# Performance work log

Hardware: AMD Instinct MI355X
Metric: run time of the kernel (lower is better)

Reference implementation:

```python
import jax, jax.numpy as jnp
import numpy as np

N = 10000      # nodes
E = 100000     # edges per direction
DIN = 128      # input feature dim (== hidden so layers stack)
H = 4          # attention heads
C = 128        # out channels per head (concat=False -> mean over heads)
ED = 16        # edge_attr dim
L = 2          # number of layers (len(hidden_sizes))
NEG_SLOPE = 0.2
EPS = 1e-5


def setup_inputs() -> dict:
    key = jax.random.key(0)
    ks = jax.random.split(key, 32)
    f32 = jnp.float32

    def nrm(k, shape, s=0.05):
        return jax.random.normal(k, shape, dtype=f32) * s

    inp = {}
    inp["x"] = nrm(ks[0], (N, DIN), 1.0)
    inp["fwd_edges_index"] = jax.random.randint(ks[1], (2, E), 0, N, dtype=jnp.int32)
    inp["bwd_edges_index"] = jax.random.randint(ks[2], (2, E), 0, N, dtype=jnp.int32)
    inp["edge_attr"] = nrm(ks[3], (E, ED), 1.0)
    # GATv2 params, stacked over layers; suffix _f = FWDGATLayer, _b = BWDGATLayer
    for i, sfx in enumerate(["f", "b"]):
        o = 4 + 7 * i
        inp[f"Wl_{sfx}"] = nrm(ks[o + 0], (L, DIN, H * C))   # lin_l (source x_j)
        inp[f"bl_{sfx}"] = jnp.zeros((L, H * C), f32)
        inp[f"Wr_{sfx}"] = nrm(ks[o + 1], (L, DIN, H * C))   # lin_r (target x_i)
        inp[f"br_{sfx}"] = jnp.zeros((L, H * C), f32)
        inp[f"We_{sfx}"] = nrm(ks[o + 2], (L, ED, H * C))    # lin_edge (no bias)
        inp[f"att_{sfx}"] = nrm(ks[o + 3], (L, H, C))        # attention vector a
        inp[f"bias_{sfx}"] = jnp.zeros((L, C), f32)          # final bias (concat=False)
    # Merge MLP: Linear(2C,C) -> ReLU -> Linear(C,C)
    inp["Wm1"] = nrm(ks[20], (L, 2 * C, C)); inp["bm1"] = jnp.zeros((L, C), f32)
    inp["Wm2"] = nrm(ks[21], (L, C, C));     inp["bm2"] = jnp.zeros((L, C), f32)
    # BatchNorm affine params (training-mode batch stats)
    inp["gamma"] = jnp.ones((L, C), f32)
    inp["beta"] = jnp.zeros((L, C), f32)
    return inp


def gatv2(x, src, dst, eattr, Wl, bl, Wr, br, We, att, bias):
    """PyG GATv2Conv, heads=H, concat=False (mean over heads), share_weights=False."""
    xl = (x @ Wl + bl).reshape(N, H, C)          # source-side transform (x_j)
    xr = (x @ Wr + br).reshape(N, H, C)          # target-side transform (x_i)
    ee = (eattr @ We).reshape(E, H, C)           # edge embedding
    z = jax.nn.leaky_relu(xl[src] + xr[dst] + ee, NEG_SLOPE)   # [E,H,C]
    logits = jnp.einsum('ehc,hc->eh', z, att)    # per-edge per-head scores
    # scatter-softmax over incoming edges of each target node
    amax = jax.lax.stop_gradient(jax.ops.segment_max(logits, dst, num_segments=N))
    amax = jnp.where(jnp.isfinite(amax), amax, 0.0)  # nodes with no in-edges
    ex = jnp.exp(logits - amax[dst])
    denom = jax.ops.segment_sum(ex, dst, num_segments=N)
    alpha = ex / denom[dst]                      # [E,H]
    msg = (xl[src] * alpha[:, :, None]).reshape(E, H * C)
    agg = jax.ops.segment_sum(msg, dst, num_segments=N).reshape(N, H, C)
    return agg.mean(axis=1) + bias               # concat=False -> head mean


def batch_norm(x, gamma, beta):
    mu = x.mean(axis=0)
    var = x.var(axis=0)  # biased var, as torch BN uses for normalization
    return gamma * (x - mu) * jax.lax.rsqrt(var + EPS) + beta


def reference(x, fwd_edges_index, bwd_edges_index, edge_attr,
              Wl_f, bl_f, Wr_f, br_f, We_f, att_f, bias_f,
              Wl_b, bl_b, Wr_b, br_b, We_b, att_b, bias_b,
              Wm1, bm1, Wm2, bm2, gamma, beta):
    fs, fd = fwd_edges_index[0], fwd_edges_index[1]
    bs, bd = bwd_edges_index[0], bwd_edges_index[1]
    h = x
    for l in range(L):
        f = gatv2(h, fs, fd, edge_attr, Wl_f[l], bl_f[l], Wr_f[l], br_f[l],
                  We_f[l], att_f[l], bias_f[l])
        b = gatv2(h, bs, bd, edge_attr, Wl_b[l], bl_b[l], Wr_b[l], br_b[l],
                  We_b[l], att_b[l], bias_b[l])
        m = jnp.concatenate([f, b], axis=1)                     # [N, 2C]
        m = jax.nn.relu(m @ Wm1[l] + bm1[l]) @ Wm2[l] + bm2[l]  # merge MLP
        h = jax.nn.relu(batch_norm(m, gamma[l], beta[l]))
    return h
```

## Files before the change

kernel.cpp:

```cpp
#include <hip/hip_runtime.h>

constexpr int N_  = 10000;
constexpr int E_  = 100000;
constexpr int HC_ = 512;
constexpr int MP_ = 10112;
constexpr float NEG_SLOPE_ = 0.2f;

typedef unsigned int u32;
typedef unsigned short u16;
typedef __attribute__((ext_vector_type(8))) short bf16x8;
typedef __attribute__((ext_vector_type(4))) float f32x4;

__device__ __forceinline__ u16 f2bf(float f) {
  u32 u = __float_as_uint(f);
  u32 r = u + 0x7fffu + ((u >> 16) & 1u);
  return (u16)(r >> 16);
}
__device__ __forceinline__ float bf2f(u16 u) {
  return __uint_as_float((u32)u << 16);
}
__device__ __forceinline__ void async16(const void* g, void* l) {
  __builtin_amdgcn_global_load_lds((const __attribute__((address_space(1))) u32*)g,
                                   (__attribute__((address_space(3))) u32*)l, 16, 0, 0);
}


__global__ void k_hist(const int* __restrict__ fdst, const int* __restrict__ bdst,
                       int* __restrict__ degf, int* __restrict__ degb) {
  int e = blockIdx.x * 256 + threadIdx.x;
  if (e < E_) {
    atomicAdd(&degf[fdst[e]], 1);
    atomicAdd(&degb[bdst[e]], 1);
  }
}

__global__ void k_scan(const int* __restrict__ degf, const int* __restrict__ degb,
                       int* __restrict__ rpf, int* __restrict__ rpb) {
  const int* deg = blockIdx.x ? degb : degf;
  int* rp = blockIdx.x ? rpb : rpf;
  const int CH = 40;
  int t = threadIdx.x;
  int base = t * CH;
  int s = 0;
  for (int i = 0; i < CH; ++i) {
    int idx = base + i;
    if (idx < N_) s += deg[idx];
  }
  __shared__ int lds[256];
  lds[t] = s;
  __syncthreads();
  for (int off = 1; off < 256; off <<= 1) {
    int v = (t >= off) ? lds[t - off] : 0;
    __syncthreads();
    lds[t] += v;
    __syncthreads();
  }
  int run = lds[t] - s;
  for (int i = 0; i < CH; ++i) {
    int idx = base + i;
    if (idx < N_) { rp[idx] = run; run += deg[idx]; }
  }
  if (t == 255) rp[N_] = lds[255];
}

__global__ void k_scatter(const int* __restrict__ src, const int* __restrict__ dst,
                          const int* __restrict__ rp, int* __restrict__ cur,
                          int* __restrict__ csrc, int* __restrict__ ceid) {
  int e = blockIdx.x * 256 + threadIdx.x;
  if (e < E_) {
    int d = dst[e];
    int pos = rp[d] + atomicAdd(&cur[d], 1);
    csrc[pos] = src[e];
    ceid[pos] = e;
  }
}


__global__ void k_wprep(const float* __restrict__ Wl_f, const float* __restrict__ Wr_f,
                        const float* __restrict__ Wl_b, const float* __restrict__ Wr_b,
                        const float* __restrict__ bl_f, const float* __restrict__ br_f,
                        const float* __restrict__ bl_b, const float* __restrict__ br_b,
                        const float* __restrict__ Wm1, const float* __restrict__ Wm2,
                        u16* __restrict__ WCATh, float* __restrict__ BCAT,
                        u16* __restrict__ WM1h, u16* __restrict__ WM2h) {
  int idx = blockIdx.x * 256 + threadIdx.x;
  if (idx < 2 * 2048 * 128) {
    int l = idx >> 18;
    int rem = idx & 262143;
    int j = rem >> 7, k = rem & 127;
    int grp = j >> 9, jj = j & 511;
    const float* W = grp == 0 ? Wl_f : grp == 1 ? Wr_f : grp == 2 ? Wl_b : Wr_b;
    WCATh[idx] = f2bf(W[((size_t)(l * 128 + k)) * 512 + jj]);
  }
  if (idx < 2 * 2048) {
    int l = idx >> 11, j = idx & 2047;
    int grp = j >> 9, jj = j & 511;
    const float* bs = grp == 0 ? bl_f : grp == 1 ? br_f : grp == 2 ? bl_b : br_b;
    BCAT[idx] = bs[l * 512 + jj];
  }
  if (idx < 2 * 128 * 256) {
    int l = idx >> 15;
    int rem = idx & 32767;
    int n = rem >> 8, k = rem & 255;
    WM1h[idx] = f2bf(Wm1[((size_t)(l * 256 + k)) * 128 + n]);
  }
  if (idx < 2 * 128 * 128) {
    int l = idx >> 14;
    int rem = idx & 16383;
    int n = rem >> 7, k = rem & 127;
    WM2h[idx] = f2bf(Wm2[((size_t)(l * 128 + k)) * 128 + n]);
  }
}

__global__ void k_cast(const float* __restrict__ x, u16* __restrict__ Xh) {
  int idx = blockIdx.x * 256 + threadIdx.x;
  if (idx >= MP_ * 32) return;
  int row = idx >> 5;
  int c4 = (idx & 31) << 2;
  ushort4 o;
  if (row < N_) {
    float4 v = *reinterpret_cast<const float4*>(x + (size_t)row * 128 + c4);
    o.x = f2bf(v.x); o.y = f2bf(v.y); o.z = f2bf(v.z); o.w = f2bf(v.w);
  } else {
    o.x = o.y = o.z = o.w = 0;
  }
  *reinterpret_cast<ushort4*>(Xh + (size_t)row * 128 + c4) = o;
}


template <int K>
__global__ __launch_bounds__(256) void k_hgemm(const u16* __restrict__ A,
                                               const u16* __restrict__ Bt,
                                               const float* __restrict__ bias,
                                               u16* __restrict__ Cb, int M, int Ncols) {
  __shared__ __align__(16) u16 As[128 * 128];
  __shared__ __align__(16) u16 Bs[128 * 128];
  const int tid = threadIdx.x;
  const int lane = tid & 63, wave = tid >> 6;
  const int l16 = lane & 15, lq = lane >> 4;
  const int wm = wave & 1, wn = wave >> 1;
  const u16* Arow0 = A + (size_t)blockIdx.y * 128 * K;
  const u16* Brow0 = Bt + (size_t)blockIdx.x * 128 * K;

  f32x4 acc[4][4];
#pragma unroll
  for (int i = 0; i < 4; ++i)
#pragma unroll
    for (int j = 0; j < 4; ++j) acc[i][j] = (f32x4){0.f, 0.f, 0.f, 0.f};

  for (int kc = 0; kc < K; kc += 128) {
    if (kc) __syncthreads();
#pragma unroll
    for (int i = 0; i < 8; ++i) {
      int rg = i * 4 + wave;
      int r = rg * 4 + (lane >> 4);
      int cc = kc + (lane & 15) * 8;
      async16(Arow0 + (size_t)r * K + cc, (char*)As + rg * 1024);
      async16(Brow0 + (size_t)r * K + cc, (char*)Bs + rg * 1024);
    }
    __syncthreads();
    const u16* Ab = As + (wm * 64 + l16) * 128 + lq * 8;
    const u16* Bb = Bs + (wn * 64 + l16) * 128 + lq * 8;
#pragma unroll
    for (int ks = 0; ks < 4; ++ks) {
      bf16x8 af[4], bfr[4];
#pragma unroll
      for (int i = 0; i < 4; ++i)
        af[i] = *reinterpret_cast<const bf16x8*>(Ab + i * 16 * 128 + ks * 32);
#pragma unroll
      for (int j = 0; j < 4; ++j)
        bfr[j] = *reinterpret_cast<const bf16x8*>(Bb + j * 16 * 128 + ks * 32);
#pragma unroll
      for (int i = 0; i < 4; ++i)
#pragma unroll
        for (int j = 0; j < 4; ++j)
          acc[i][j] = __builtin_amdgcn_mfma_f32_16x16x32_bf16(af[i], bfr[j], acc[i][j], 0, 0, 0);
    }
  }

  const int row_base = blockIdx.y * 128 + wm * 64;
  const int col_base = blockIdx.x * 128 + wn * 64;
#pragma unroll
  for (int i = 0; i < 4; ++i) {
#pragma unroll
    for (int r = 0; r < 4; ++r) {
      int row = row_base + i * 16 + lq * 4 + r;
      if (row < M) {
#pragma unroll
        for (int j = 0; j < 4; ++j) {
          int col = col_base + j * 16 + l16;
          Cb[(size_t)row * Ncols + col] = f2bf(acc[i][j][r] + bias[col]);
        }
      }
    }
  }
}


__global__ __launch_bounds__(128) void k_gat(
    const u16* __restrict__ XLXRh, const float* __restrict__ eattr,
    const int* __restrict__ rpf, const int* __restrict__ csf, const int* __restrict__ cef,
    const int* __restrict__ rpb, const int* __restrict__ csb, const int* __restrict__ ceb,
    const float* __restrict__ We_f, const float* __restrict__ We_b,
    const float* __restrict__ att_f, const float* __restrict__ att_b,
    const float* __restrict__ bias_f, const float* __restrict__ bias_b,
    u16* __restrict__ FBh, int layer) {
  const int n = blockIdx.x;
  const int dir = blockIdx.y;
  const int* rp = dir ? rpb : rpf;
  const int* cs = dir ? csb : csf;
  const int* ce = dir ? ceb : cef;
  const float* We = (dir ? We_b : We_f) + layer * 16 * HC_;
  const float* att = (dir ? att_b : att_f) + layer * HC_;
  const float* bias = (dir ? bias_b : bias_f) + layer * 128;
  const int t = threadIdx.x;
  const int ch = t << 2;
  const u16* XL = XLXRh + dir * 1024;
  const u16* XR = XL + 512;

  float4 a4 = *reinterpret_cast<const float4*>(att + ch);
  ushort4 xru = *reinterpret_cast<const ushort4*>(XR + (size_t)n * 2048 + ch);
  float xrx = bf2f(xru.x), xry = bf2f(xru.y), xrz = bf2f(xru.z), xrw = bf2f(xru.w);
  float4 we[16];
#pragma unroll
  for (int k = 0; k < 16; ++k)
    we[k] = *reinterpret_cast<const float4*>(We + k * HC_ + ch);

  auto pre = [&](float xx, float xy, float xz, float xw,
                 float4 e0, float4 e1, float4 e2, float4 e3) -> float {
    float zx = xx + xrx, zy = xy + xry, zz = xz + xrz, zw = xw + xrw;
#define EE_(c, kk)                  \
  zx = fmaf(c, we[kk].x, zx);       \
  zy = fmaf(c, we[kk].y, zy);       \
  zz = fmaf(c, we[kk].z, zz);       \
  zw = fmaf(c, we[kk].w, zw)
    EE_(e0.x, 0); EE_(e0.y, 1); EE_(e0.z, 2); EE_(e0.w, 3);
    EE_(e1.x, 4); EE_(e1.y, 5); EE_(e1.z, 6); EE_(e1.w, 7);
    EE_(e2.x, 8); EE_(e2.y, 9); EE_(e2.z, 10); EE_(e2.w, 11);
    EE_(e3.x, 12); EE_(e3.y, 13); EE_(e3.z, 14); EE_(e3.w, 15);
#undef EE_
    float lx = zx > 0.f ? zx : NEG_SLOPE_ * zx;
    float ly = zy > 0.f ? zy : NEG_SLOPE_ * zy;
    float lz = zz > 0.f ? zz : NEG_SLOPE_ * zz;
    float lw = zw > 0.f ? zw : NEG_SLOPE_ * zw;
    return fmaf(lx, a4.x, fmaf(ly, a4.y, fmaf(lz, a4.z, lw * a4.w)));
  };

  float accx = 0.f, accy = 0.f, accz = 0.f, accw = 0.f;
  float denom = 0.f;
  const int s = rp[n], epos = rp[n + 1];
  int i = s;
  for (; i + 2 <= epos; i += 2) {
    int sn0 = cs[i], sn1 = cs[i + 1];
    int ei0 = ce[i], ei1 = ce[i + 1];
    ushort4 xu0 = *reinterpret_cast<const ushort4*>(XL + (size_t)sn0 * 2048 + ch);
    ushort4 xu1 = *reinterpret_cast<const ushort4*>(XL + (size_t)sn1 * 2048 + ch);
    const float4* p0 = reinterpret_cast<const float4*>(eattr + (size_t)ei0 * 16);
    const float4* p1 = reinterpret_cast<const float4*>(eattr + (size_t)ei1 * 16);
    float4 A0 = p0[0], A1 = p0[1], A2 = p0[2], A3 = p0[3];
    float4 B0 = p1[0], B1 = p1[1], B2 = p1[2], B3 = p1[3];
    float x00 = bf2f(xu0.x), x01 = bf2f(xu0.y), x02 = bf2f(xu0.z), x03 = bf2f(xu0.w);
    float x10 = bf2f(xu1.x), x11 = bf2f(xu1.y), x12 = bf2f(xu1.z), x13 = bf2f(xu1.w);
    float pA = pre(x00, x01, x02, x03, A0, A1, A2, A3);
    float pB = pre(x10, x11, x12, x13, B0, B1, B2, B3);
#pragma unroll
    for (int kk = 1; kk < 32; kk <<= 1) {
      pA += __shfl_xor(pA, kk, 32);
      pB += __shfl_xor(pB, kk, 32);
    }
    float ex0 = __expf(pA);
    float ex1 = __expf(pB);
    denom += ex0 + ex1;
    accx = fmaf(ex0, x00, fmaf(ex1, x10, accx));
    accy = fmaf(ex0, x01, fmaf(ex1, x11, accy));
    accz = fmaf(ex0, x02, fmaf(ex1, x12, accz));
    accw = fmaf(ex0, x03, fmaf(ex1, x13, accw));
  }
  if (i < epos) {
    int sn0 = cs[i], ei0 = ce[i];
    ushort4 xu0 = *reinterpret_cast<const ushort4*>(XL + (size_t)sn0 * 2048 + ch);
    const float4* p0 = reinterpret_cast<const float4*>(eattr + (size_t)ei0 * 16);
    float4 A0 = p0[0], A1 = p0[1], A2 = p0[2], A3 = p0[3];
    float x00 = bf2f(xu0.x), x01 = bf2f(xu0.y), x02 = bf2f(xu0.z), x03 = bf2f(xu0.w);
    float pA = pre(x00, x01, x02, x03, A0, A1, A2, A3);
#pragma unroll
    for (int kk = 1; kk < 32; kk <<= 1) pA += __shfl_xor(pA, kk, 32);
    float ex0 = __expf(pA);
    denom += ex0;
    accx = fmaf(ex0, x00, accx);
    accy = fmaf(ex0, x01, accy);
    accz = fmaf(ex0, x02, accz);
    accw = fmaf(ex0, x03, accw);
  }

  __shared__ __align__(16) float red[512];
  float inv = denom > 0.f ? 1.f / denom : 0.f;
  red[ch] = accx * inv;
  red[ch + 1] = accy * inv;
  red[ch + 2] = accz * inv;
  red[ch + 3] = accw * inv;
  __syncthreads();
  if (t < 32) {
    int c = t << 2;
    float4 r0 = *reinterpret_cast<const float4*>(&red[c]);
    float4 r1 = *reinterpret_cast<const float4*>(&red[c + 128]);
    float4 r2 = *reinterpret_cast<const float4*>(&red[c + 256]);
    float4 r3 = *reinterpret_cast<const float4*>(&red[c + 384]);
    float4 b4 = *reinterpret_cast<const float4*>(bias + c);
    ushort4 o;
    o.x = f2bf(0.25f * (r0.x + r1.x + r2.x + r3.x) + b4.x);
    o.y = f2bf(0.25f * (r0.y + r1.y + r2.y + r3.y) + b4.y);
    o.z = f2bf(0.25f * (r0.z + r1.z + r2.z + r3.z) + b4.z);
    o.w = f2bf(0.25f * (r0.w + r1.w + r2.w + r3.w) + b4.w);
    *reinterpret_cast<ushort4*>(FBh + (size_t)n * 256 + dir * 128 + c) = o;
  }
}


__global__ __launch_bounds__(256) void k_mlp(const u16* __restrict__ FBh,
                                             const u16* __restrict__ W1,
                                             const float* __restrict__ b1,
                                             const u16* __restrict__ W2,
                                             const float* __restrict__ b2,
                                             float* __restrict__ M2,
                                             float* __restrict__ STATS) {
  __shared__ __align__(16) u16 As[128 * 128];
  __shared__ __align__(16) u16 Bs[64 * 128];
  __shared__ __align__(16) u16 M1s[64 * 128];
  __shared__ float ls[256];
  const int tid = threadIdx.x;
  const int lane = tid & 63, wave = tid >> 6;
  const int l16 = lane & 15, lq = lane >> 4;
  const int mb = blockIdx.x * 64;

  const int wr = wave & 1, wc = wave >> 1;
  f32x4 acc1[4][2];
#pragma unroll
  for (int i = 0; i < 4; ++i)
#pragma unroll
    for (int j = 0; j < 2; ++j) acc1[i][j] = (f32x4){0.f, 0.f, 0.f, 0.f};

  for (int kc = 0; kc < 256; kc += 128) {
    if (kc) __syncthreads();
#pragma unroll
    for (int tI = 0; tI < 8; ++tI) {
      int rg = tI * 4 + wave;
      int r = rg * 4 + (lane >> 4);
      async16(W1 + (size_t)r * 256 + kc + (lane & 15) * 8, (char*)As + rg * 1024);
    }
#pragma unroll
    for (int tI = 0; tI < 4; ++tI) {
      int rg = tI * 4 + wave;
      int r = rg * 4 + (lane >> 4);
      async16(FBh + (size_t)(mb + r) * 256 + kc + (lane & 15) * 8, (char*)Bs + rg * 1024);
    }
    __syncthreads();
#pragma unroll
    for (int ks = 0; ks < 4; ++ks) {
      bf16x8 af[4], bfv[2];
#pragma unroll
      for (int i = 0; i < 4; ++i)
        af[i] = *reinterpret_cast<const bf16x8*>(As + (wr * 64 + i * 16 + l16) * 128 + ks * 32 + lq * 8);
#pragma unroll
      for (int j = 0; j < 2; ++j)
        bfv[j] = *reinterpret_cast<const bf16x8*>(Bs + (wc * 32 + j * 16 + l16) * 128 + ks * 32 + lq * 8);
#pragma unroll
      for (int i = 0; i < 4; ++i)
#pragma unroll
        for (int j = 0; j < 2; ++j)
          acc1[i][j] = __builtin_amdgcn_mfma_f32_16x16x32_bf16(af[i], bfv[j], acc1[i][j], 0, 0, 0);
    }
  }
  ls[tid] = 0.f;
#pragma unroll
  for (int i = 0; i < 4; ++i) {
    float4 b1v = *reinterpret_cast<const float4*>(b1 + wr * 64 + i * 16 + lq * 4);
    float bb[4] = {b1v.x, b1v.y, b1v.z, b1v.w};
#pragma unroll
    for (int j = 0; j < 2; ++j) {
      int m = wc * 32 + j * 16 + l16;
      int k2 = wr * 64 + i * 16 + lq * 4;
      ushort4 o;
      o.x = f2bf(fmaxf(acc1[i][j][0] + bb[0], 0.f));
      o.y = f2bf(fmaxf(acc1[i][j][1] + bb[1], 0.f));
      o.z = f2bf(fmaxf(acc1[i][j][2] + bb[2], 0.f));
      o.w = f2bf(fmaxf(acc1[i][j][3] + bb[3], 0.f));
      *reinterpret_cast<ushort4*>(M1s + m * 128 + k2) = o;
    }
  }
  __syncthreads();
#pragma unroll
  for (int tI = 0; tI < 8; ++tI) {
    int rg = tI * 4 + wave;
    int r = rg * 4 + (lane >> 4);
    async16(W2 + (size_t)r * 128 + (lane & 15) * 8, (char*)As + rg * 1024);
  }
  __syncthreads();

  const int wr2 = wave & 1, wc2 = wave >> 1;
  f32x4 acc2[2][4];
#pragma unroll
  for (int i = 0; i < 2; ++i)
#pragma unroll
    for (int j = 0; j < 4; ++j) acc2[i][j] = (f32x4){0.f, 0.f, 0.f, 0.f};
#pragma unroll
  for (int ks = 0; ks < 4; ++ks) {
    bf16x8 af2[2], bf2v[4];
#pragma unroll
    for (int i = 0; i < 2; ++i)
      af2[i] = *reinterpret_cast<const bf16x8*>(M1s + (wr2 * 32 + i * 16 + l16) * 128 + ks * 32 + lq * 8);
#pragma unroll
    for (int j = 0; j < 4; ++j)
      bf2v[j] = *reinterpret_cast<const bf16x8*>(As + (wc2 * 64 + j * 16 + l16) * 128 + ks * 32 + lq * 8);
#pragma unroll
    for (int i = 0; i < 2; ++i)
#pragma unroll
      for (int j = 0; j < 4; ++j)
        acc2[i][j] = __builtin_amdgcn_mfma_f32_16x16x32_bf16(af2[i], bf2v[j], acc2[i][j], 0, 0, 0);
  }

  float s1[4] = {0.f, 0.f, 0.f, 0.f}, s2[4] = {0.f, 0.f, 0.f, 0.f};
  float b2j[4];
#pragma unroll
  for (int j = 0; j < 4; ++j) b2j[j] = b2[wc2 * 64 + j * 16 + l16];
#pragma unroll
  for (int i = 0; i < 2; ++i) {
#pragma unroll
    for (int r = 0; r < 4; ++r) {
      int m = mb + wr2 * 32 + i * 16 + lq * 4 + r;
      if (m < N_) {
#pragma unroll
        for (int j = 0; j < 4; ++j) {
          float v = acc2[i][j][r] + b2j[j];
          M2[(size_t)m * 128 + wc2 * 64 + j * 16 + l16] = v;
          s1[j] += v;
          s2[j] = fmaf(v, v, s2[j]);
        }
      }
    }
  }
#pragma unroll
  for (int j = 0; j < 4; ++j) {
    int c = wc2 * 64 + j * 16 + l16;
    atomicAdd(&ls[c], s1[j]);
    atomicAdd(&ls[128 + c], s2[j]);
  }
  __syncthreads();
  if (tid < 128) {
    atomicAdd(&STATS[tid], ls[tid]);
    atomicAdd(&STATS[128 + tid], ls[128 + tid]);
  }
}


__global__ void k_bn(const float* __restrict__ m2, const float* __restrict__ stats,
                     const float* __restrict__ gamma, const float* __restrict__ beta,
                     u16* __restrict__ houth, float* __restrict__ outf) {
  int idx = blockIdx.x * 256 + threadIdx.x;
  if (idx >= N_ * 32) return;
  int n = idx >> 5;
  int c = (idx & 31) << 2;
  float4 v = *reinterpret_cast<const float4*>(m2 + (size_t)n * 128 + c);
  const float invN = 1.f / (float)N_;
  float o[4];
  float vv[4] = {v.x, v.y, v.z, v.w};
#pragma unroll
  for (int q = 0; q < 4; ++q) {
    float mu = stats[c + q] * invN;
    float var = stats[128 + c + q] * invN - mu * mu;
    float rs = rsqrtf(var + 1e-5f);
    o[q] = fmaxf(gamma[c + q] * (vv[q] - mu) * rs + beta[c + q], 0.f);
  }
  ushort4 oh;
  oh.x = f2bf(o[0]); oh.y = f2bf(o[1]); oh.z = f2bf(o[2]); oh.w = f2bf(o[3]);
  *reinterpret_cast<ushort4*>(houth + (size_t)n * 128 + c) = oh;
  if (outf) {
    float4 of = make_float4(o[0], o[1], o[2], o[3]);
    *reinterpret_cast<float4*>(outf + (size_t)n * 128 + c) = of;
  }
}


extern "C" void kernel_launch(void* const* d_in, const int* in_sizes, int n_in,
                              void* d_out, int out_size, void* d_ws, size_t ws_size,
                              hipStream_t stream) {
  (void)in_sizes; (void)n_in; (void)out_size; (void)ws_size;
  const float* x      = (const float*)d_in[0];
  const int*   fwd    = (const int*)d_in[1];
  const int*   bwd    = (const int*)d_in[2];
  const float* eattr  = (const float*)d_in[3];
  const float* Wl_f   = (const float*)d_in[4];
  const float* bl_f   = (const float*)d_in[5];
  const float* Wr_f   = (const float*)d_in[6];
  const float* br_f   = (const float*)d_in[7];
  const float* We_f   = (const float*)d_in[8];
  const float* att_f  = (const float*)d_in[9];
  const float* bias_f = (const float*)d_in[10];
  const float* Wl_b   = (const float*)d_in[11];
  const float* bl_b   = (const float*)d_in[12];
  const float* Wr_b   = (const float*)d_in[13];
  const float* br_b   = (const float*)d_in[14];
  const float* We_b   = (const float*)d_in[15];
  const float* att_b  = (const float*)d_in[16];
  const float* bias_b = (const float*)d_in[17];
  const float* Wm1    = (const float*)d_in[18];
  const float* bm1    = (const float*)d_in[19];
  const float* Wm2    = (const float*)d_in[20];
  const float* bm2    = (const float*)d_in[21];
  const float* gamma  = (const float*)d_in[22];
  const float* beta   = (const float*)d_in[23];

  char* ws = (char*)d_ws;
  size_t off = 0;
  auto take = [&](size_t bytes) -> char* {
    char* p = ws + off;
    off += (bytes + 255) & ~(size_t)255;
    return p;
  };
  u16* WCATh = (u16*)take(2ull * 2048 * 128 * 2);
  float* BCAT = (float*)take(2ull * 2048 * 4);
  u16* WM1h = (u16*)take(2ull * 128 * 256 * 2);
  u16* WM2h = (u16*)take(2ull * 128 * 128 * 2);
  u16* Xh    = (u16*)take((size_t)MP_ * 128 * 2);
  u16* HBh   = (u16*)take((size_t)MP_ * 128 * 2);
  u16* XLXRh = (u16*)take((size_t)MP_ * 2048 * 2);
  u16* FBh   = (u16*)take((size_t)MP_ * 256 * 2);
  float* M2  = (float*)take((size_t)MP_ * 128 * 4);
  int* DEGS  = (int*)take(4ull * 40192);
  int* degf = DEGS;
  int* degb = DEGS + (40192 / 4);
  int* curf = DEGS + 2 * (40192 / 4);
  int* curb = DEGS + 3 * (40192 / 4);
  int* rpf = (int*)take((N_ + 1) * 4);
  int* rpb = (int*)take((N_ + 1) * 4);
  int* csf = (int*)take((size_t)E_ * 4);
  int* cef = (int*)take((size_t)E_ * 4);
  int* csb = (int*)take((size_t)E_ * 4);
  int* ceb = (int*)take((size_t)E_ * 4);
  float* STATS = (float*)take(256 * 4);

  hipMemsetAsync(DEGS, 0, 4ull * 40192, stream);
  k_wprep<<<2048, 256, 0, stream>>>(Wl_f, Wr_f, Wl_b, Wr_b, bl_f, br_f, bl_b, br_b,
                                    Wm1, Wm2, WCATh, BCAT, WM1h, WM2h);
  k_cast<<<(MP_ * 32 + 255) / 256, 256, 0, stream>>>(x, Xh);
  k_hist<<<(E_ + 255) / 256, 256, 0, stream>>>(fwd + E_, bwd + E_, degf, degb);
  k_scan<<<2, 256, 0, stream>>>(degf, degb, rpf, rpb);
  k_scatter<<<(E_ + 255) / 256, 256, 0, stream>>>(fwd, fwd + E_, rpf, curf, csf, cef);
  k_scatter<<<(E_ + 255) / 256, 256, 0, stream>>>(bwd, bwd + E_, rpb, curb, csb, ceb);

  for (int l = 0; l < 2; ++l) {
    const u16* hin = (l == 0) ? Xh : HBh;
    k_hgemm<128><<<dim3(16, MP_ / 128), 256, 0, stream>>>(
        hin, WCATh + (size_t)l * 2048 * 128, BCAT + l * 2048, XLXRh, N_, 2048);
    k_gat<<<dim3(N_, 2), 128, 0, stream>>>(XLXRh, eattr, rpf, csf, cef, rpb, csb, ceb,
                                           We_f, We_b, att_f, att_b, bias_f, bias_b, FBh, l);
    hipMemsetAsync(STATS, 0, 256 * 4, stream);
    k_mlp<<<MP_ / 64, 256, 0, stream>>>(FBh, WM1h + (size_t)l * 128 * 256, bm1 + l * 128,
                                        WM2h + (size_t)l * 128 * 128, bm2 + l * 128, M2, STATS);
    k_bn<<<(N_ * 32 + 255) / 256, 256, 0, stream>>>(
        M2, STATS, gamma + l * 128, beta + l * 128, HBh, (l == 1) ? (float*)d_out : nullptr);
  }
}
```

Measured before the change: 398.5 us.

## Permute edge attributes into CSR order and use packed float2 FMAs in GAT

The scatter kernel now writes each edge's 16-float attribute vector into a CSR-ordered buffer, so the GAT kernel reads edge features contiguously instead of gathering them through an edge-id indirection. The GAT inner math is rewritten with 2-wide float vectors so the compiler can emit packed FMA instructions, and launch bounds ask for higher occupancy. Separately, the per-layer stats memsets are folded into the initial degree memset. The cost is an extra 12.8 MB permuted copy of the edge attributes in setup, plus possible register pressure from the occupancy hint.

```diff
diff --git a/kernel.cpp b/kernel.cpp
--- a/kernel.cpp
+++ b/kernel.cpp
@@ -10,6 +10,7 @@
 typedef unsigned short u16;
 typedef __attribute__((ext_vector_type(8))) short bf16x8;
 typedef __attribute__((ext_vector_type(4))) float f32x4;
+typedef __attribute__((ext_vector_type(2))) float f32x2;
 
 __device__ __forceinline__ u16 f2bf(float f) {
   u32 u = __float_as_uint(f);
@@ -22,6 +23,12 @@
 __device__ __forceinline__ void async16(const void* g, void* l) {
   __builtin_amdgcn_global_load_lds((const __attribute__((address_space(1))) u32*)g,
                                    (__attribute__((address_space(3))) u32*)l, 16, 0, 0);
+}
+__device__ __forceinline__ f32x2 fma2s(float c, f32x2 v, f32x2 acc) {
+  return __builtin_elementwise_fma((f32x2){c, c}, v, acc);
+}
+__device__ __forceinline__ f32x2 fma2v(f32x2 a, f32x2 b, f32x2 acc) {
+  return __builtin_elementwise_fma(a, b, acc);
 }
 
 
@@ -65,13 +72,16 @@
 
 __global__ void k_scatter(const int* __restrict__ src, const int* __restrict__ dst,
                           const int* __restrict__ rp, int* __restrict__ cur,
-                          int* __restrict__ csrc, int* __restrict__ ceid) {
+                          int* __restrict__ csrc, float* __restrict__ eP,
+                          const float* __restrict__ eattr) {
   int e = blockIdx.x * 256 + threadIdx.x;
   if (e < E_) {
     int d = dst[e];
     int pos = rp[d] + atomicAdd(&cur[d], 1);
     csrc[pos] = src[e];
-    ceid[pos] = e;
+    const float4* s4 = reinterpret_cast<const float4*>(eattr + (size_t)e * 16);
+    float4* d4 = reinterpret_cast<float4*>(eP + (size_t)pos * 16);
+    d4[0] = s4[0]; d4[1] = s4[1]; d4[2] = s4[2]; d4[3] = s4[3];
   }
 }
 
@@ -197,10 +207,10 @@
 }
 
 
-__global__ __launch_bounds__(128) void k_gat(
-    const u16* __restrict__ XLXRh, const float* __restrict__ eattr,
-    const int* __restrict__ rpf, const int* __restrict__ csf, const int* __restrict__ cef,
-    const int* __restrict__ rpb, const int* __restrict__ csb, const int* __restrict__ ceb,
+__global__ __launch_bounds__(128, 4) void k_gat(
+    const u16* __restrict__ XLXRh,
+    const int* __restrict__ rpf, const int* __restrict__ csf, const float* __restrict__ ePf,
+    const int* __restrict__ rpb, const int* __restrict__ csb, const float* __restrict__ ePb,
     const float* __restrict__ We_f, const float* __restrict__ We_b,
     const float* __restrict__ att_f, const float* __restrict__ att_b,
     const float* __restrict__ bias_f, const float* __restrict__ bias_b,
@@ -209,7 +219,7 @@
   const int dir = blockIdx.y;
   const int* rp = dir ? rpb : rpf;
   const int* cs = dir ? csb : csf;
-  const int* ce = dir ? ceb : cef;
+  const float* eP = dir ? ePb : ePf;
   const float* We = (dir ? We_b : We_f) + layer * 16 * HC_;
   const float* att = (dir ? att_b : att_f) + layer * HC_;
   const float* bias = (dir ? bias_b : bias_f) + layer * 128;
@@ -218,51 +228,52 @@
   const u16* XL = XLXRh + dir * 1024;
   const u16* XR = XL + 512;
 
-  float4 a4 = *reinterpret_cast<const float4*>(att + ch);
+  float4 av = *reinterpret_cast<const float4*>(att + ch);
+  f32x2 a01 = {av.x, av.y}, a23 = {av.z, av.w};
   ushort4 xru = *reinterpret_cast<const ushort4*>(XR + (size_t)n * 2048 + ch);
-  float xrx = bf2f(xru.x), xry = bf2f(xru.y), xrz = bf2f(xru.z), xrw = bf2f(xru.w);
-  float4 we[16];
-#pragma unroll
-  for (int k = 0; k < 16; ++k)
-    we[k] = *reinterpret_cast<const float4*>(We + k * HC_ + ch);
-
-  auto pre = [&](float xx, float xy, float xz, float xw,
-                 float4 e0, float4 e1, float4 e2, float4 e3) -> float {
-    float zx = xx + xrx, zy = xy + xry, zz = xz + xrz, zw = xw + xrw;
+  f32x2 xr01 = {bf2f(xru.x), bf2f(xru.y)}, xr23 = {bf2f(xru.z), bf2f(xru.w)};
+  f32x2 we0[16], we1[16];
+#pragma unroll
+  for (int k = 0; k < 16; ++k) {
+    float4 w = *reinterpret_cast<const float4*>(We + k * HC_ + ch);
+    we0[k] = (f32x2){w.x, w.y};
+    we1[k] = (f32x2){w.z, w.w};
+  }
+
+  auto pre = [&](f32x2 x01, f32x2 x23, const float4* ep) -> float {
+    float4 e0 = ep[0], e1 = ep[1], e2 = ep[2], e3 = ep[3];
+    f32x2 z01 = x01 + xr01, z23 = x23 + xr23;
 #define EE_(c, kk)                  \
-  zx = fmaf(c, we[kk].x, zx);       \
-  zy = fmaf(c, we[kk].y, zy);       \
-  zz = fmaf(c, we[kk].z, zz);       \
-  zw = fmaf(c, we[kk].w, zw)
+  z01 = fma2s(c, we0[kk], z01);     \
+  z23 = fma2s(c, we1[kk], z23)
     EE_(e0.x, 0); EE_(e0.y, 1); EE_(e0.z, 2); EE_(e0.w, 3);
     EE_(e1.x, 4); EE_(e1.y, 5); EE_(e1.z, 6); EE_(e1.w, 7);
     EE_(e2.x, 8); EE_(e2.y, 9); EE_(e2.z, 10); EE_(e2.w, 11);
     EE_(e3.x, 12); EE_(e3.y, 13); EE_(e3.z, 14); EE_(e3.w, 15);
 #undef EE_
-    float lx = zx > 0.f ? zx : NEG_SLOPE_ * zx;
-    float ly = zy > 0.f ? zy : NEG_SLOPE_ * zy;
-    float lz = zz > 0.f ? zz : NEG_SLOPE_ * zz;
-    float lw = zw > 0.f ? zw : NEG_SLOPE_ * zw;
-    return fmaf(lx, a4.x, fmaf(ly, a4.y, fmaf(lz, a4.z, lw * a4.w)));
+    const f32x2 zz = {0.f, 0.f};
+    const f32x2 ns = {NEG_SLOPE_, NEG_SLOPE_};
+    f32x2 l01 = fma2v(ns, __builtin_elementwise_min(z01, zz),
+                      __builtin_elementwise_max(z01, zz));
+    f32x2 l23 = fma2v(ns, __builtin_elementwise_min(z23, zz),
+                      __builtin_elementwise_max(z23, zz));
+    f32x2 d = fma2v(l01, a01, l23 * a23);
+    return d.x + d.y;
   };
 
-  float accx = 0.f, accy = 0.f, accz = 0.f, accw = 0.f;
+  f32x2 acc01 = {0.f, 0.f}, acc23 = {0.f, 0.f};
   float denom = 0.f;
   const int s = rp[n], epos = rp[n + 1];
   int i = s;
   for (; i + 2 <= epos; i += 2) {
     int sn0 = cs[i], sn1 = cs[i + 1];
-    int ei0 = ce[i], ei1 = ce[i + 1];
     ushort4 xu0 = *reinterpret_cast<const ushort4*>(XL + (size_t)sn0 * 2048 + ch);
     ushort4 xu1 = *reinterpret_cast<const ushort4*>(XL + (size_t)sn1 * 2048 + ch);
-    const float4* p0 = reinterpret_cast<const float4*>(eattr + (size_t)ei0 * 16);
-    const float4* p1 = reinterpret_cast<const float4*>(eattr + (size_t)ei1 * 16);
-    float4 A0 = p0[0], A1 = p0[1], A2 = p0[2], A3 = p0[3];
-    float4 B0 = p1[0], B1 = p1[1], B2 = p1[2], B3 = p1[3];
-    float x00 = bf2f(xu0.x), x01 = bf2f(xu0.y), x02 = bf2f(xu0.z), x03 = bf2f(xu0.w);
-    float x10 = bf2f(xu1.x), x11 = bf2f(xu1.y), x12 = bf2f(xu1.z), x13 = bf2f(xu1.w);
-    float pA = pre(x00, x01, x02, x03, A0, A1, A2, A3);
-    float pB = pre(x10, x11, x12, x13, B0, B1, B2, B3);
+    const float4* p0 = reinterpret_cast<const float4*>(eP + (size_t)i * 16);
+    f32x2 x001 = {bf2f(xu0.x), bf2f(xu0.y)}, x023 = {bf2f(xu0.z), bf2f(xu0.w)};
+    f32x2 x101 = {bf2f(xu1.x), bf2f(xu1.y)}, x123 = {bf2f(xu1.z), bf2f(xu1.w)};
+    float pA = pre(x001, x023, p0);
+    float pB = pre(x101, x123, p0 + 4);
 #pragma unroll
     for (int kk = 1; kk < 32; kk <<= 1) {
       pA += __shfl_xor(pA, kk, 32);
@@ -271,34 +282,29 @@
     float ex0 = __expf(pA);
     float ex1 = __expf(pB);
     denom += ex0 + ex1;
-    accx = fmaf(ex0, x00, fmaf(ex1, x10, accx));
-    accy = fmaf(ex0, x01, fmaf(ex1, x11, accy));
-    accz = fmaf(ex0, x02, fmaf(ex1, x12, accz));
-    accw = fmaf(ex0, x03, fmaf(ex1, x13, accw));
+    acc01 = fma2s(ex0, x001, fma2s(ex1, x101, acc01));
+    acc23 = fma2s(ex0, x023, fma2s(ex1, x123, acc23));
   }
   if (i < epos) {
-    int sn0 = cs[i], ei0 = ce[i];
+    int sn0 = cs[i];
     ushort4 xu0 = *reinterpret_cast<const ushort4*>(XL + (size_t)sn0 * 2048 + ch);
-    const float4* p0 = reinterpret_cast<const float4*>(eattr + (size_t)ei0 * 16);
-    float4 A0 = p0[0], A1 = p0[1], A2 = p0[2], A3 = p0[3];
-    float x00 = bf2f(xu0.x), x01 = bf2f(xu0.y), x02 = bf2f(xu0.z), x03 = bf2f(xu0.w);
-    float pA = pre(x00, x01, x02, x03, A0, A1, A2, A3);
+    const float4* p0 = reinterpret_cast<const float4*>(eP + (size_t)i * 16);
+    f32x2 x001 = {bf2f(xu0.x), bf2f(xu0.y)}, x023 = {bf2f(xu0.z), bf2f(xu0.w)};
+    float pA = pre(x001, x023, p0);
 #pragma unroll
     for (int kk = 1; kk < 32; kk <<= 1) pA += __shfl_xor(pA, kk, 32);
     float ex0 = __expf(pA);
     denom += ex0;
-    accx = fmaf(ex0, x00, accx);
-    accy = fmaf(ex0, x01, accy);
-    accz = fmaf(ex0, x02, accz);
-    accw = fmaf(ex0, x03, accw);
+    acc01 = fma2s(ex0, x001, acc01);
+    acc23 = fma2s(ex0, x023, acc23);
   }
 
   __shared__ __align__(16) float red[512];
   float inv = denom > 0.f ? 1.f / denom : 0.f;
-  red[ch] = accx * inv;
-  red[ch + 1] = accy * inv;
-  red[ch + 2] = accz * inv;
-  red[ch + 3] = accw * inv;
+  red[ch] = acc01.x * inv;
+  red[ch + 1] = acc01.y * inv;
+  red[ch + 2] = acc23.x * inv;
+  red[ch + 3] = acc23.y * inv;
   __syncthreads();
   if (t < 32) {
     int c = t << 2;
@@ -527,6 +533,7 @@
   u16* FBh   = (u16*)take((size_t)MP_ * 256 * 2);
   float* M2  = (float*)take((size_t)MP_ * 128 * 4);
   int* DEGS  = (int*)take(4ull * 40192);
+  float* STATS = (float*)take(2ull * 256 * 4);
   int* degf = DEGS;
   int* degb = DEGS + (40192 / 4);
   int* curf = DEGS + 2 * (40192 / 4);
@@ -534,30 +541,30 @@
   int* rpf = (int*)take((N_ + 1) * 4);
   int* rpb = (int*)take((N_ + 1) * 4);
   int* csf = (int*)take((size_t)E_ * 4);
-  int* cef = (int*)take((size_t)E_ * 4);
   int* csb = (int*)take((size_t)E_ * 4);
-  int* ceb = (int*)take((size_t)E_ * 4);
-  float* STATS = (float*)take(256 * 4);
-
-  hipMemsetAsync(DEGS, 0, 4ull * 40192, stream);
+  float* ePf = (float*)take((size_t)E_ * 16 * 4);
+  float* ePb = (float*)take((size_t)E_ * 16 * 4);
+
+  hipMemsetAsync(DEGS, 0, 4ull * 40192 + 2ull * 256 * 4, stream);
   k_wprep<<<2048, 256, 0, stream>>>(Wl_f, Wr_f, Wl_b, Wr_b, bl_f, br_f, bl_b, br_b,
                                     Wm1, Wm2, WCATh, BCAT, WM1h, WM2h);
   k_cast<<<(MP_ * 32 + 255) / 256, 256, 0, stream>>>(x, Xh);
   k_hist<<<(E_ + 255) / 256, 256, 0, stream>>>(fwd + E_, bwd + E_, degf, degb);
   k_scan<<<2, 256, 0, stream>>>(degf, degb, rpf, rpb);
-  k_scatter<<<(E_ + 255) / 256, 256, 0, stream>>>(fwd, fwd + E_, rpf, curf, csf, cef);
-  k_scatter<<<(E_ + 255) / 256, 256, 0, stream>>>(bwd, bwd + E_, rpb, curb, csb, ceb);
+  k_scatter<<<(E_ + 255) / 256, 256, 0, stream>>>(fwd, fwd + E_, rpf, curf, csf, ePf, eattr);
+  k_scatter<<<(E_ + 255) / 256, 256, 0, stream>>>(bwd, bwd + E_, rpb, curb, csb, ePb, eattr);
 
   for (int l = 0; l < 2; ++l) {
     const u16* hin = (l == 0) ? Xh : HBh;
     k_hgemm<128><<<dim3(16, MP_ / 128), 256, 0, stream>>>(
         hin, WCATh + (size_t)l * 2048 * 128, BCAT + l * 2048, XLXRh, N_, 2048);
-    k_gat<<<dim3(N_, 2), 128, 0, stream>>>(XLXRh, eattr, rpf, csf, cef, rpb, csb, ceb,
+    k_gat<<<dim3(N_, 2), 128, 0, stream>>>(XLXRh, rpf, csf, ePf, rpb, csb, ePb,
                                            We_f, We_b, att_f, att_b, bias_f, bias_b, FBh, l);
-    hipMemsetAsync(STATS, 0, 256 * 4, stream);
     k_mlp<<<MP_ / 64, 256, 0, stream>>>(FBh, WM1h + (size_t)l * 128 * 256, bm1 + l * 128,
-                                        WM2h + (size_t)l * 128 * 128, bm2 + l * 128, M2, STATS);
+                                        WM2h + (size_t)l * 128 * 128, bm2 + l * 128, M2,
+                                        STATS + l * 256);
     k_bn<<<(N_ * 32 + 255) / 256, 256, 0, stream>>>(
-        M2, STATS, gamma + l * 128, beta + l * 128, HBh, (l == 1) ? (float*)d_out : nullptr);
-  }
-}
+        M2, STATS + l * 256, gamma + l * 128, beta + l * 128, HBh,
+        (l == 1) ? (float*)d_out : nullptr);
+  }
+}
```

Measured after the change: 401.3 us. Within noise of the previous version (+0.7%).
